# Kernel optimization log

Measured on AMD Instinct MI355X. Metric: run time of the kernel, lower is better.

Reference implementation:

```python
import jax, jax.numpy as jnp
import numpy as np

INPUT_DIM = 4096
OUTPUT_DIM = 4096
N_MAG_BITS = 3  # inference_sequence = [0, 3]: magnitude bits 0..2, sign bit at index 3
N_TOKENS = 8192
DESIRED_STD = np.sqrt(2.0 / INPUT_DIM)  # kaiming fan_in std target


def _ste(hard, soft):
    # straight-through estimator: forward = hard, backward = identity on soft
    return soft + jax.lax.stop_gradient(hard - soft)


def to_bit(x):
    # latent float -> {0,1} bit plane
    return _ste((x >= 0).astype(x.dtype), x)


def to_sign(x):
    # latent float -> {-1,+1} sign plane
    return _ste(jnp.where(x >= 0, 1.0, -1.0).astype(x.dtype), x)


def setup_inputs() -> dict:
    key = jax.random.key(0)
    k1, k2, k3 = jax.random.split(key, 3)
    x = jax.random.normal(k1, (N_TOKENS, INPUT_DIM), dtype=jnp.float32)
    mag = jax.random.normal(k2, (N_MAG_BITS, INPUT_DIM, OUTPUT_DIM), dtype=jnp.float32)
    sign_bit = jax.random.normal(k3, (INPUT_DIM, OUTPUT_DIM), dtype=jnp.float32)
    return {"x": x, "mag": mag, "sign_bit": sign_bit}


def reference(x, mag, sign_bit):
    # calculate_number: reconstruct weight from bit planes
    # w = sign * sum_i bit_i * 2^{-(i+1)}
    bits = to_bit(mag)  # [K, in, out]
    place = (2.0 ** -(jnp.arange(1, N_MAG_BITS + 1, dtype=jnp.float32)))  # [K]
    magnitude = jnp.einsum("kio,k->io", bits, place)
    w = to_sign(sign_bit) * magnitude  # [in, out]
    # calc_scaling_factor on detached weight (cpu/numpy round-trip in original -> constant)
    alpha = DESIRED_STD / (jnp.std(jax.lax.stop_gradient(w)) + 1e-12)
    w = w * alpha
    # F.linear(x, W.T) == x @ W
    return jnp.matmul(x, w)
```

## Files before the change

### kernel.cpp

```cpp
#include <hip/hip_runtime.h>
#include <hip/hip_bf16.h>
#include <cstdint>
#include <cstddef>

#define IN_DIM 4096
#define OUT_DIM 4096
#define NTOK 8192
#define PLANE (IN_DIM * OUT_DIM)
#define NPACK_BLOCKS 4096

#define BM 256
#define BN 256
#define BK 64
#define KTILES (IN_DIM / BK)

typedef int i32x4_t __attribute__((ext_vector_type(4)));

__device__ inline void async_load16(void* lds, const void* g) {
    __builtin_amdgcn_global_load_lds(
        (const __attribute__((address_space(1))) char*)g,
        (__attribute__((address_space(3))) char*)lds,
        16, 0, 0);
}

__global__ __launch_bounds__(256) void pack_kernel(const float* __restrict__ mag,
                                                   const float* __restrict__ sgn,
                                                   signed char* __restrict__ wT,
                                                   int* __restrict__ partials) {
    __shared__ short tile[64 * 68];
    __shared__ int red2[4], reds[4];
    const int t = threadIdx.x;
    const int o0 = blockIdx.x * 64, i0 = blockIdx.y * 64;
    const int oq = t & 15, ir = t >> 4;
    int lk2 = 0, lsk = 0;
    #pragma unroll
    for (int r = 0; r < 4; ++r) {
        const int ilo = r * 16 + ir;
        const size_t idx = (size_t)(i0 + ilo) * OUT_DIM + o0 + oq * 4;
        const float4 m0 = *(const float4*)(mag + idx);
        const float4 m1 = *(const float4*)(mag + idx + (size_t)PLANE);
        const float4 m2 = *(const float4*)(mag + idx + 2 * (size_t)PLANE);
        const float4 sv = *(const float4*)(sgn + idx);
        short4 c;
        {
            int k = ((m0.x >= 0.f) ? 4 : 0) | ((m1.x >= 0.f) ? 2 : 0) | ((m2.x >= 0.f) ? 1 : 0);
            int cd = (sv.x >= 0.f) ? k : -k; lk2 += k * k; lsk += cd; c.x = (short)cd;
        }
        {
            int k = ((m0.y >= 0.f) ? 4 : 0) | ((m1.y >= 0.f) ? 2 : 0) | ((m2.y >= 0.f) ? 1 : 0);
            int cd = (sv.y >= 0.f) ? k : -k; lk2 += k * k; lsk += cd; c.y = (short)cd;
        }
        {
            int k = ((m0.z >= 0.f) ? 4 : 0) | ((m1.z >= 0.f) ? 2 : 0) | ((m2.z >= 0.f) ? 1 : 0);
            int cd = (sv.z >= 0.f) ? k : -k; lk2 += k * k; lsk += cd; c.z = (short)cd;
        }
        {
            int k = ((m0.w >= 0.f) ? 4 : 0) | ((m1.w >= 0.f) ? 2 : 0) | ((m2.w >= 0.f) ? 1 : 0);
            int cd = (sv.w >= 0.f) ? k : -k; lk2 += k * k; lsk += cd; c.w = (short)cd;
        }
        *(short4*)&tile[ilo * 68 + oq * 4] = c;
    }
    #pragma unroll
    for (int off = 32; off > 0; off >>= 1) {
        lk2 += __shfl_down(lk2, off);
        lsk += __shfl_down(lsk, off);
    }
    const int wv = t >> 6, ln = t & 63;
    if (ln == 0) { red2[wv] = lk2; reds[wv] = lsk; }
    __syncthreads();
    if (t == 0) {
        const int bid = blockIdx.y * gridDim.x + blockIdx.x;
        partials[bid] = red2[0] + red2[1] + red2[2] + red2[3];
        partials[NPACK_BLOCKS + bid] = reds[0] + reds[1] + reds[2] + reds[3];
    }
    const int iq = t & 15, orr = t >> 4;
    #pragma unroll
    for (int r = 0; r < 4; ++r) {
        const int olo = r * 16 + orr;
        char4 w4;
        w4.x = (signed char)tile[(iq * 4 + 0) * 68 + olo];
        w4.y = (signed char)tile[(iq * 4 + 1) * 68 + olo];
        w4.z = (signed char)tile[(iq * 4 + 2) * 68 + olo];
        w4.w = (signed char)tile[(iq * 4 + 3) * 68 + olo];
        *(char4*)&wT[(size_t)(o0 + olo) * IN_DIM + i0 + iq * 4] = w4;
    }
}

__global__ __launch_bounds__(256) void alpha_kernel(const int* __restrict__ partials,
                                                    float* __restrict__ alpha8) {
    __shared__ int red2[4], reds[4];
    const int t = threadIdx.x;
    int k2 = 0, sk = 0;
    for (int i = t; i < NPACK_BLOCKS; i += 256) {
        k2 += partials[i];
        sk += partials[NPACK_BLOCKS + i];
    }
    #pragma unroll
    for (int off = 32; off > 0; off >>= 1) {
        k2 += __shfl_down(k2, off);
        sk += __shfl_down(sk, off);
    }
    const int wv = t >> 6, ln = t & 63;
    if (ln == 0) { red2[wv] = k2; reds[wv] = sk; }
    __syncthreads();
    if (t == 0) {
        const double n = (double)PLANE;
        const double sumk2 = (double)(red2[0] + red2[1] + red2[2] + red2[3]);
        const double sumsk = (double)(reds[0] + reds[1] + reds[2] + reds[3]);
        const double mean = sumsk / (8.0 * n);
        const double e2 = sumk2 / (64.0 * n);
        const double sd = sqrt(e2 - mean * mean);
        *alpha8 = (float)(sqrt(2.0 / (double)IN_DIM) / (sd + 1e-12) * 0.125);
    }
}

__global__ __launch_bounds__(256) void quant_kernel(const float* __restrict__ x,
                                                    signed char* __restrict__ xq,
                                                    float* __restrict__ steps) {
    __shared__ float red[4];
    const int r = blockIdx.x, t = threadIdx.x;
    const float* xr = x + (size_t)r * IN_DIM;
    float4 v[4];
    float am = 0.f;
    #pragma unroll
    for (int p = 0; p < 4; ++p) {
        v[p] = ((const float4*)xr)[p * 256 + t];
        am = fmaxf(am, fmaxf(fmaxf(fabsf(v[p].x), fabsf(v[p].y)),
                             fmaxf(fabsf(v[p].z), fabsf(v[p].w))));
    }
    #pragma unroll
    for (int off = 32; off > 0; off >>= 1) am = fmaxf(am, __shfl_down(am, off));
    const int wv = t >> 6, ln = t & 63;
    if (ln == 0) red[wv] = am;
    __syncthreads();
    am = fmaxf(fmaxf(red[0], red[1]), fmaxf(red[2], red[3]));
    am = fmaxf(am, 1e-30f);
    const float rstep = 127.0f / am;
    if (t == 0) steps[r] = am * (1.0f / 127.0f);
    int* xqi = (int*)(xq + (size_t)r * IN_DIM);
    #pragma unroll
    for (int p = 0; p < 4; ++p) {
        const int q0 = (int)rintf(v[p].x * rstep);
        const int q1 = (int)rintf(v[p].y * rstep);
        const int q2 = (int)rintf(v[p].z * rstep);
        const int q3 = (int)rintf(v[p].w * rstep);
        xqi[p * 256 + t] = (q0 & 0xFF) | ((q1 & 0xFF) << 8) | ((q2 & 0xFF) << 16) | (q3 << 24);
    }
}

__global__ __launch_bounds__(1024, 4) void gemm_kernel(const signed char* __restrict__ A,
                                                       const signed char* __restrict__ B,
                                                       float* __restrict__ C,
                                                       const float* __restrict__ alphap,
                                                       const float* __restrict__ steps) {
    __shared__ __align__(16) signed char As[4][BM * BK];
    __shared__ __align__(16) signed char Bs[4][BN * BK];
    const int t = threadIdx.x;
    const int lane = t & 63;
    const int wave = t >> 6;
    const int wm = wave >> 2, wn = wave & 3;
    const int r15 = lane & 15, q = lane >> 4;

    const int raw = blockIdx.x;
    const int wg = (raw & 7) * 64 + (raw >> 3);
    const int m0 = (wg >> 4) * BM;
    const int n0 = (wg & 15) * BN;

    int aoff[4], boff[4];
    #pragma unroll
    for (int i = 0; i < 4; ++i) {
        const int r = wm * 64 + i * 16 + r15;
        aoff[i] = r * BK + ((q ^ ((r >> 1) & 3)) << 4);
    }
    #pragma unroll
    for (int i = 0; i < 4; ++i) {
        const int r = wn * 64 + i * 16 + r15;
        boff[i] = r * BK + ((q ^ ((r >> 1) & 3)) << 4);
    }

    const int ra = t >> 2;
    const int sc = (((t & 3) ^ ((t >> 3) & 3)) << 4);
    const size_t srcA = (size_t)(m0 + ra) * IN_DIM + sc;
    const size_t srcB = (size_t)(n0 + ra) * IN_DIM + sc;

    i32x4_t acc[4][4] = {};

#define STAGE(kt, buf) do {                                          \
        const int koff_ = (kt) * BK;                                 \
        async_load16(&As[buf][t * 16], A + srcA + koff_);            \
        async_load16(&Bs[buf][t * 16], B + srcB + koff_);            \
    } while (0)

#define COMPUTE(buf) do {                                            \
        i32x4_t a_[4], b_[4];                                        \
        _Pragma("unroll")                                            \
        for (int i = 0; i < 4; ++i)                                  \
            a_[i] = *(const i32x4_t*)&As[buf][aoff[i]];              \
        _Pragma("unroll")                                            \
        for (int i = 0; i < 4; ++i)                                  \
            b_[i] = *(const i32x4_t*)&Bs[buf][boff[i]];              \
        __builtin_amdgcn_s_setprio(1);                               \
        _Pragma("unroll")                                            \
        for (int mt = 0; mt < 4; ++mt)                               \
            _Pragma("unroll")                                        \
            for (int nt = 0; nt < 4; ++nt)                           \
                acc[mt][nt] = __builtin_amdgcn_mfma_i32_16x16x64_i8( \
                    a_[mt], b_[nt], acc[mt][nt], 0, 0, 0);           \
        __builtin_amdgcn_s_setprio(0);                               \
    } while (0)

    STAGE(0, 0); STAGE(1, 1); STAGE(2, 2);

    #pragma unroll 4
    for (int kt = 0; kt < KTILES - 3; ++kt) {
        STAGE(kt + 3, (kt + 3) & 3);
        asm volatile("s_waitcnt vmcnt(6)" ::: "memory");
        __builtin_amdgcn_s_barrier();
        COMPUTE(kt & 3);
        __builtin_amdgcn_s_barrier();
    }
    asm volatile("s_waitcnt vmcnt(4)" ::: "memory");
    __builtin_amdgcn_s_barrier();
    COMPUTE((KTILES - 3) & 3);
    __builtin_amdgcn_s_barrier();
    asm volatile("s_waitcnt vmcnt(2)" ::: "memory");
    __builtin_amdgcn_s_barrier();
    COMPUTE((KTILES - 2) & 3);
    __builtin_amdgcn_s_barrier();
    asm volatile("s_waitcnt vmcnt(0)" ::: "memory");
    __builtin_amdgcn_s_barrier();
    COMPUTE((KTILES - 1) & 3);

#undef COMPUTE
#undef STAGE

    const float alpha8 = *alphap;
    #pragma unroll
    for (int mt = 0; mt < 4; ++mt) {
        const int mbase = m0 + wm * 64 + mt * 16 + q * 4;
        const float s0 = alpha8 * steps[mbase + 0];
        const float s1 = alpha8 * steps[mbase + 1];
        const float s2 = alpha8 * steps[mbase + 2];
        const float s3 = alpha8 * steps[mbase + 3];
        #pragma unroll
        for (int nt = 0; nt < 4; ++nt) {
            const int n = n0 + wn * 64 + nt * 16 + r15;
            float* cp = C + (size_t)mbase * OUT_DIM + n;
            cp[0 * OUT_DIM] = (float)acc[mt][nt][0] * s0;
            cp[1 * OUT_DIM] = (float)acc[mt][nt][1] * s1;
            cp[2 * OUT_DIM] = (float)acc[mt][nt][2] * s2;
            cp[3 * OUT_DIM] = (float)acc[mt][nt][3] * s3;
        }
    }
}

extern "C" void kernel_launch(void* const* d_in, const int* in_sizes, int n_in,
                              void* d_out, int out_size, void* d_ws, size_t ws_size,
                              hipStream_t stream) {
    const float* x   = (const float*)d_in[0];
    const float* mag = (const float*)d_in[1];
    const float* sgn = (const float*)d_in[2];
    float* out = (float*)d_out;

    char* ws = (char*)d_ws;
    int* partials = (int*)ws;
    float* alphap = (float*)(ws + 32768);
    float* steps  = (float*)(ws + 65536);
    signed char* wT = (signed char*)(ws + 131072);
    signed char* xq = (signed char*)(ws + 131072 + (size_t)PLANE);

    pack_kernel<<<dim3(OUT_DIM / 64, IN_DIM / 64), 256, 0, stream>>>(mag, sgn, wT, partials);
    quant_kernel<<<NTOK, 256, 0, stream>>>(x, xq, steps);
    alpha_kernel<<<1, 256, 0, stream>>>(partials, alphap);
    gemm_kernel<<<dim3((NTOK / BM) * (OUT_DIM / BN)), 1024, 0, stream>>>(xq, wT, out, alphap, steps);
}
```

Before: 551.6 us.

## Switch int8 GEMM to 32x32x32 MFMA tiles and repad pack transpose tile

Replaces the 16x16x64 int8 MFMA with the 32x32x32 variant, so each wave computes 2x2 tiles of 32x32 with 16-element accumulators. LDS fragment offsets and the epilogue row mapping are rewritten to match the new lane layout. The aim is fewer LDS fragment loads per MFMA and higher per-instruction throughput. It also changes the pack kernel's shared tile pitch from 68 to 66 shorts with split short2 stores, to alter LDS bank conflicts in the transpose. The new epilogue writes columns with a row stride that may coalesce differently.

```diff
diff --git a/kernel.cpp b/kernel.cpp
--- a/kernel.cpp
+++ b/kernel.cpp
@@ -14,7 +14,8 @@
 #define BK 64
 #define KTILES (IN_DIM / BK)
 
-typedef int i32x4_t __attribute__((ext_vector_type(4)));
+typedef int i32x4_t  __attribute__((ext_vector_type(4)));
+typedef int i32x16_t __attribute__((ext_vector_type(16)));
 
 __device__ inline void async_load16(void* lds, const void* g) {
     __builtin_amdgcn_global_load_lds(
@@ -27,7 +28,7 @@
                                                    const float* __restrict__ sgn,
                                                    signed char* __restrict__ wT,
                                                    int* __restrict__ partials) {
-    __shared__ short tile[64 * 68];
+    __shared__ short tile[64 * 66];
     __shared__ int red2[4], reds[4];
     const int t = threadIdx.x;
     const int o0 = blockIdx.x * 64, i0 = blockIdx.y * 64;
@@ -58,7 +59,10 @@
             int k = ((m0.w >= 0.f) ? 4 : 0) | ((m1.w >= 0.f) ? 2 : 0) | ((m2.w >= 0.f) ? 1 : 0);
             int cd = (sv.w >= 0.f) ? k : -k; lk2 += k * k; lsk += cd; c.w = (short)cd;
         }
-        *(short4*)&tile[ilo * 68 + oq * 4] = c;
+        short2 lo, hi;
+        lo.x = c.x; lo.y = c.y; hi.x = c.z; hi.y = c.w;
+        *(short2*)&tile[ilo * 66 + oq * 4]     = lo;
+        *(short2*)&tile[ilo * 66 + oq * 4 + 2] = hi;
     }
     #pragma unroll
     for (int off = 32; off > 0; off >>= 1) {
@@ -78,10 +82,10 @@
     for (int r = 0; r < 4; ++r) {
         const int olo = r * 16 + orr;
         char4 w4;
-        w4.x = (signed char)tile[(iq * 4 + 0) * 68 + olo];
-        w4.y = (signed char)tile[(iq * 4 + 1) * 68 + olo];
-        w4.z = (signed char)tile[(iq * 4 + 2) * 68 + olo];
-        w4.w = (signed char)tile[(iq * 4 + 3) * 68 + olo];
+        w4.x = (signed char)tile[(iq * 4 + 0) * 66 + olo];
+        w4.y = (signed char)tile[(iq * 4 + 1) * 66 + olo];
+        w4.z = (signed char)tile[(iq * 4 + 2) * 66 + olo];
+        w4.w = (signed char)tile[(iq * 4 + 3) * 66 + olo];
         *(char4*)&wT[(size_t)(o0 + olo) * IN_DIM + i0 + iq * 4] = w4;
     }
 }
@@ -159,31 +163,37 @@
     const int lane = t & 63;
     const int wave = t >> 6;
     const int wm = wave >> 2, wn = wave & 3;
-    const int r15 = lane & 15, q = lane >> 4;
+    const int ln = lane & 31, hi = lane >> 5;
 
     const int raw = blockIdx.x;
     const int wg = (raw & 7) * 64 + (raw >> 3);
     const int m0 = (wg >> 4) * BM;
     const int n0 = (wg & 15) * BN;
 
-    int aoff[4], boff[4];
-    #pragma unroll
-    for (int i = 0; i < 4; ++i) {
-        const int r = wm * 64 + i * 16 + r15;
-        aoff[i] = r * BK + ((q ^ ((r >> 1) & 3)) << 4);
-    }
-    #pragma unroll
-    for (int i = 0; i < 4; ++i) {
-        const int r = wn * 64 + i * 16 + r15;
-        boff[i] = r * BK + ((q ^ ((r >> 1) & 3)) << 4);
-    }
+    int aoff[2][2], boff[2][2];
+    #pragma unroll
+    for (int mt = 0; mt < 2; ++mt)
+        #pragma unroll
+        for (int ks = 0; ks < 2; ++ks) {
+            const int r = wm * 64 + mt * 32 + ln;
+            const int c = ks * 2 + hi;
+            aoff[mt][ks] = r * BK + ((c ^ ((r >> 1) & 3)) << 4);
+        }
+    #pragma unroll
+    for (int nt = 0; nt < 2; ++nt)
+        #pragma unroll
+        for (int ks = 0; ks < 2; ++ks) {
+            const int r = wn * 64 + nt * 32 + ln;
+            const int c = ks * 2 + hi;
+            boff[nt][ks] = r * BK + ((c ^ ((r >> 1) & 3)) << 4);
+        }
 
     const int ra = t >> 2;
     const int sc = (((t & 3) ^ ((t >> 3) & 3)) << 4);
     const size_t srcA = (size_t)(m0 + ra) * IN_DIM + sc;
     const size_t srcB = (size_t)(n0 + ra) * IN_DIM + sc;
 
-    i32x4_t acc[4][4] = {};
+    i32x16_t acc[2][2] = {};
 
 #define STAGE(kt, buf) do {                                          \
         const int koff_ = (kt) * BK;                                 \
@@ -192,20 +202,26 @@
     } while (0)
 
 #define COMPUTE(buf) do {                                            \
-        i32x4_t a_[4], b_[4];                                        \
+        i32x4_t a_[2][2], b_[2][2];                                  \
         _Pragma("unroll")                                            \
-        for (int i = 0; i < 4; ++i)                                  \
-            a_[i] = *(const i32x4_t*)&As[buf][aoff[i]];              \
+        for (int mt = 0; mt < 2; ++mt)                               \
+            _Pragma("unroll")                                        \
+            for (int ks = 0; ks < 2; ++ks)                           \
+                a_[mt][ks] = *(const i32x4_t*)&As[buf][aoff[mt][ks]];\
         _Pragma("unroll")                                            \
-        for (int i = 0; i < 4; ++i)                                  \
-            b_[i] = *(const i32x4_t*)&Bs[buf][boff[i]];              \
+        for (int nt = 0; nt < 2; ++nt)                               \
+            _Pragma("unroll")                                        \
+            for (int ks = 0; ks < 2; ++ks)                           \
+                b_[nt][ks] = *(const i32x4_t*)&Bs[buf][boff[nt][ks]];\
         __builtin_amdgcn_s_setprio(1);                               \
         _Pragma("unroll")                                            \
-        for (int mt = 0; mt < 4; ++mt)                               \
+        for (int ks = 0; ks < 2; ++ks)                               \
             _Pragma("unroll")                                        \
-            for (int nt = 0; nt < 4; ++nt)                           \
-                acc[mt][nt] = __builtin_amdgcn_mfma_i32_16x16x64_i8( \
-                    a_[mt], b_[nt], acc[mt][nt], 0, 0, 0);           \
+            for (int mt = 0; mt < 2; ++mt)                           \
+                _Pragma("unroll")                                    \
+                for (int nt = 0; nt < 2; ++nt)                       \
+                    acc[mt][nt] = __builtin_amdgcn_mfma_i32_32x32x32_i8( \
+                        a_[mt][ks], b_[nt][ks], acc[mt][nt], 0, 0, 0);   \
         __builtin_amdgcn_s_setprio(0);                               \
     } while (0)
 
@@ -236,20 +252,17 @@
 
     const float alpha8 = *alphap;
     #pragma unroll
-    for (int mt = 0; mt < 4; ++mt) {
-        const int mbase = m0 + wm * 64 + mt * 16 + q * 4;
-        const float s0 = alpha8 * steps[mbase + 0];
-        const float s1 = alpha8 * steps[mbase + 1];
-        const float s2 = alpha8 * steps[mbase + 2];
-        const float s3 = alpha8 * steps[mbase + 3];
+    for (int mt = 0; mt < 2; ++mt) {
+        const int mrow0 = m0 + wm * 64 + mt * 32 + 4 * hi;
         #pragma unroll
-        for (int nt = 0; nt < 4; ++nt) {
-            const int n = n0 + wn * 64 + nt * 16 + r15;
-            float* cp = C + (size_t)mbase * OUT_DIM + n;
-            cp[0 * OUT_DIM] = (float)acc[mt][nt][0] * s0;
-            cp[1 * OUT_DIM] = (float)acc[mt][nt][1] * s1;
-            cp[2 * OUT_DIM] = (float)acc[mt][nt][2] * s2;
-            cp[3 * OUT_DIM] = (float)acc[mt][nt][3] * s3;
+        for (int nt = 0; nt < 2; ++nt) {
+            const int n = n0 + wn * 64 + nt * 32 + ln;
+            #pragma unroll
+            for (int j = 0; j < 16; ++j) {
+                const int mrow = mrow0 + (j & 3) + 8 * (j >> 2);
+                C[(size_t)mrow * OUT_DIM + n] =
+                    (float)acc[mt][nt][j] * (alpha8 * steps[mrow]);
+            }
         }
     }
 }
```

After: 562.8 us. 2.0% more time.
